# Kernel optimization log

Measured on AMD Instinct MI355X. Metric: run time of the kernel, lower is better.

## Reference

```python
import jax, jax.numpy as jnp
import numpy as np

B, N, DIN, DOUT = 8, 2048, 128, 128

def setup_inputs() -> dict:
    key = jax.random.key(0)
    k1, k2, k3, k4 = jax.random.split(key, 4)
    x = jax.random.normal(k1, (B, N, DIN), dtype=jnp.float32)
    adj = jax.random.uniform(k2, (B, N, N), dtype=jnp.float32)
    W = jax.random.normal(k3, (DIN, DOUT), dtype=jnp.float32) / np.sqrt(DIN)
    b = jax.random.normal(k4, (DOUT,), dtype=jnp.float32) * 0.01
    return {"x": x, "adj": adj, "W": W, "b": b}

def reference(x, adj, W, b):
    # degree over last dim of adj: [B, N]
    degree = jnp.sum(adj, axis=2)
    d_norm = 1.0 / jnp.sqrt(degree + 1e-8)
    # D^{-1/2} A D^{-1/2} == row/col elementwise scaling (same math as diag_embed+bmm)
    adj_norm = d_norm[:, :, None] * adj * d_norm[:, None, :]
    support = jnp.einsum('bnm,bmd->bnd', adj_norm, x)  # [B, N, DIN]
    return support @ W + b  # [B, N, DOUT]
```

## Files before the change

### kernel.cpp

```cpp
#include <hip/hip_runtime.h>
#include <hip/hip_bf16.h>

#define NN 2048
#define DD 128

typedef __attribute__((ext_vector_type(4))) float f32x4;
typedef __attribute__((ext_vector_type(8))) short short8;
typedef __attribute__((ext_vector_type(2))) unsigned int u32x2;

__device__ __forceinline__ unsigned short f2bf_bits(float f) {
  union { __hip_bfloat16 h; unsigned short s; } u;
  u.h = __float2bfloat16(f);
  return u.s;
}

__device__ __forceinline__ short8 cvt8(f32x4 a, f32x4 b) {
  short8 r;
  r[0] = (short)f2bf_bits(a[0]); r[1] = (short)f2bf_bits(a[1]);
  r[2] = (short)f2bf_bits(a[2]); r[3] = (short)f2bf_bits(a[3]);
  r[4] = (short)f2bf_bits(b[0]); r[5] = (short)f2bf_bits(b[1]);
  r[6] = (short)f2bf_bits(b[2]); r[7] = (short)f2bf_bits(b[3]);
  return r;
}

__device__ __forceinline__ void gld16(const void* src, void* lds) {
  __builtin_amdgcn_global_load_lds(
      (const __attribute__((address_space(1))) void*)src,
      (__attribute__((address_space(3))) void*)lds, 16, 0, 0);
}

__global__ void k_degcvt(const float* __restrict__ adj, float* __restrict__ dnorm,
                         short* __restrict__ adjS) {
  const int wv = threadIdx.x >> 6;
  const int ln = threadIdx.x & 63;
  const int row = blockIdx.x * 4 + wv;
  const f32x4* rowp = (const f32x4*)(adj + (size_t)row * NN);
  f32x4 v[8];
  float s = 0.0f;
#pragma unroll
  for (int i = 0; i < 8; ++i) {
    v[i] = rowp[i * 64 + ln];
    s += v[i][0] + v[i][1] + v[i][2] + v[i][3];
  }
#pragma unroll
  for (int off = 32; off >= 1; off >>= 1) s += __shfl_xor(s, off);
  const float dn = rsqrtf(s + 1e-8f);
  if (ln == 0) dnorm[row] = dn;
  u32x2* orow = (u32x2*)(adjS + (size_t)row * NN);
#pragma unroll
  for (int i = 0; i < 8; ++i) {
    u32x2 u;
    u[0] = (unsigned)f2bf_bits(v[i][0] * dn) | ((unsigned)f2bf_bits(v[i][1] * dn) << 16);
    u[1] = (unsigned)f2bf_bits(v[i][2] * dn) | ((unsigned)f2bf_bits(v[i][3] * dn) << 16);
    orow[i * 64 + ln] = u;
  }
}

__global__ void k_y(const float* __restrict__ x, const float* __restrict__ W,
                    const float* __restrict__ dnorm, short* __restrict__ yT) {
  const int ln = threadIdx.x & 63;
  const int wv = threadIdx.x >> 6;
  const int bb = blockIdx.x >> 5;
  const int n0 = (blockIdx.x & 31) << 6;
  const int l15 = ln & 15, l4 = ln >> 4;
  const int dbase = wv * 32;

  short8 af[2][4];
#pragma unroll
  for (int dt = 0; dt < 2; ++dt)
#pragma unroll
    for (int ks = 0; ks < 4; ++ks) {
      short8 a;
#pragma unroll
      for (int j = 0; j < 8; ++j)
        a[j] = (short)f2bf_bits(W[(size_t)(ks * 32 + l4 * 8 + j) * DD + dbase + dt * 16 + l15]);
      af[dt][ks] = a;
    }

  f32x4 acc[2][4];
#pragma unroll
  for (int dt = 0; dt < 2; ++dt)
#pragma unroll
    for (int nt = 0; nt < 4; ++nt) acc[dt][nt] = (f32x4)0.0f;

  const float* xb = x + (size_t)bb * NN * DD;
  const float* dnb = dnorm + (size_t)bb * NN;
#pragma unroll
  for (int nt = 0; nt < 4; ++nt) {
    const int n = n0 + nt * 16 + l15;
    const float dn = dnb[n];
#pragma unroll
    for (int ks = 0; ks < 4; ++ks) {
      f32x4 p = *(const f32x4*)(xb + (size_t)n * DD + ks * 32 + l4 * 8);
      f32x4 q = *(const f32x4*)(xb + (size_t)n * DD + ks * 32 + l4 * 8 + 4);
      short8 bf = cvt8(p * dn, q * dn);
#pragma unroll
      for (int dt = 0; dt < 2; ++dt)
        acc[dt][nt] = __builtin_amdgcn_mfma_f32_16x16x32_bf16(af[dt][ks], bf, acc[dt][nt], 0, 0, 0);
    }
  }

  short* yb = yT + (size_t)bb * DD * NN;
#pragma unroll
  for (int dt = 0; dt < 2; ++dt)
#pragma unroll
    for (int nt = 0; nt < 4; ++nt)
#pragma unroll
      for (int r = 0; r < 4; ++r) {
        int d = dbase + dt * 16 + l4 * 4 + r;
        yb[(size_t)d * NN + n0 + nt * 16 + l15] = (short)f2bf_bits(acc[dt][nt][r]);
      }
}

__launch_bounds__(512, 1)
__global__ void k_gemm(const short* __restrict__ adjS, const short* __restrict__ yT,
                       const float* __restrict__ bias, float* __restrict__ out) {
  __shared__ short As[6][4096];

  const int t = threadIdx.x;
  const int ln = t & 63;
  const int wv = t >> 6;
  const int orig = ((blockIdx.x & 7) << 5) | (blockIdx.x >> 3);
  const int bb = orig >> 5;
  const int m0 = (orig & 31) << 6;

  const char* ablk = (const char*)(adjS + ((size_t)bb * NN + m0) * NN);
  const int oc = (wv << 4) + (ln & 15);
  const int kg8 = (ln >> 4) << 3;
  const short* ybase = yT + ((size_t)bb * DD + oc) * NN;

  f32x4 acc[4];
#pragma unroll
  for (int m = 0; m < 4; ++m) acc[m] = (f32x4)0.0f;

  auto stage = [&](int tile, int buf) {
    unsigned L = (unsigned)t << 4;
    unsigned row = L >> 7;
    unsigned off = L & 127u;
    unsigned soff = off ^ ((row & 7u) << 4);
    const char* src = ablk + (size_t)row * (NN * 2) + (size_t)tile * 128 + soff;
    gld16(src, (char*)As + buf * 8192 + L);
  };
  auto loadB = [&](int tile, int ks) {
    return *(const short8*)(ybase + tile * 64 + ks * 32 + kg8);
  };
  auto compute = [&](int buf, short8 bk0, short8 bk1) {
    const char* base = (const char*)As + buf * 8192;
#pragma unroll
    for (int ks = 0; ks < 2; ++ks) {
      short8 bf = ks ? bk1 : bk0;
#pragma unroll
      for (int m = 0; m < 4; ++m) {
        unsigned row = (unsigned)(m * 16 + (ln & 15));
        unsigned c = (unsigned)(ks * 64 + (ln >> 4) * 16);
        short8 a = *(const short8*)(base + (row << 7) + (c ^ ((row & 7u) << 4)));
        acc[m] = __builtin_amdgcn_mfma_f32_16x16x32_bf16(a, bf, acc[m], 0, 0, 0);
      }
    }
  };

#pragma unroll
  for (int p = 0; p < 5; ++p) stage(p, p);
  short8 b0k0 = loadB(0, 0), b0k1 = loadB(0, 1);
  short8 b1k0 = loadB(1, 0), b1k1 = loadB(1, 1);
  asm volatile("s_waitcnt vmcnt(0)\n\ts_barrier" ::: "memory");

  int cbuf = 0, sbuf = 5;
  for (int tt = 0; tt < 32; tt += 2) {
    stage((tt + 5) & 31, sbuf);
    short8 n0k0 = loadB((tt + 2) & 31, 0), n0k1 = loadB((tt + 2) & 31, 1);
    compute(cbuf, b0k0, b0k1);
    asm volatile("s_waitcnt vmcnt(12)\n\ts_barrier" ::: "memory");
    cbuf = (cbuf == 5) ? 0 : cbuf + 1;
    sbuf = (sbuf == 5) ? 0 : sbuf + 1;
    stage((tt + 6) & 31, sbuf);
    short8 n1k0 = loadB((tt + 3) & 31, 0), n1k1 = loadB((tt + 3) & 31, 1);
    compute(cbuf, b1k0, b1k1);
    asm volatile("s_waitcnt vmcnt(12)\n\ts_barrier" ::: "memory");
    cbuf = (cbuf == 5) ? 0 : cbuf + 1;
    sbuf = (sbuf == 5) ? 0 : sbuf + 1;
    b0k0 = n0k0; b0k1 = n0k1; b1k0 = n1k0; b1k1 = n1k1;
  }

  const float bv = bias[oc];
  const int rbase = (ln >> 4) << 2;
#pragma unroll
  for (int m = 0; m < 4; ++m)
#pragma unroll
    for (int r = 0; r < 4; ++r)
      out[(size_t)(bb * NN + m0 + m * 16 + rbase + r) * DD + oc] = acc[m][r] + bv;
}

extern "C" void kernel_launch(void* const* d_in, const int* in_sizes, int n_in,
                              void* d_out, int out_size, void* d_ws, size_t ws_size,
                              hipStream_t stream) {
  (void)in_sizes; (void)n_in; (void)out_size; (void)ws_size;
  const float* x = (const float*)d_in[0];
  const float* adj = (const float*)d_in[1];
  const float* W = (const float*)d_in[2];
  const float* bias = (const float*)d_in[3];
  float* out = (float*)d_out;

  char* ws = (char*)d_ws;
  float* dnorm = (float*)ws;
  short* yT = (short*)(ws + (1 << 16));
  short* adjS = (short*)(ws + (1 << 16) + (4 << 20));

  k_degcvt<<<4096, 256, 0, stream>>>(adj, dnorm, adjS);
  k_y<<<256, 256, 0, stream>>>(x, W, dnorm, yT);
  k_gemm<<<256, 512, 0, stream>>>(adjS, yT, bias, out);
}
```

Before: 71.91 us.

## Fuse adj bf16 conversion into GEMM and apply row normalization in epilogue

Drops the intermediate bf16 copy of the normalized adjacency. The degree kernel now only computes d^{-1/2}, and the GEMM reads fp32 adj directly, converts it to bf16 while writing LDS, and applies row scaling to the output. This removes a 64MB write plus its reread, at the cost of reading fp32 adj twice and a register-staged, per-tile-barrier pipeline with smaller 32-row tiles and more blocks.

```diff
diff --git a/kernel.cpp b/kernel.cpp
--- a/kernel.cpp
+++ b/kernel.cpp
@@ -23,37 +23,20 @@
   return r;
 }
 
-__device__ __forceinline__ void gld16(const void* src, void* lds) {
-  __builtin_amdgcn_global_load_lds(
-      (const __attribute__((address_space(1))) void*)src,
-      (__attribute__((address_space(3))) void*)lds, 16, 0, 0);
-}
-
-__global__ void k_degcvt(const float* __restrict__ adj, float* __restrict__ dnorm,
-                         short* __restrict__ adjS) {
+__global__ void k_degree(const float* __restrict__ adj, float* __restrict__ dnorm) {
   const int wv = threadIdx.x >> 6;
   const int ln = threadIdx.x & 63;
   const int row = blockIdx.x * 4 + wv;
   const f32x4* rowp = (const f32x4*)(adj + (size_t)row * NN);
-  f32x4 v[8];
   float s = 0.0f;
 #pragma unroll
   for (int i = 0; i < 8; ++i) {
-    v[i] = rowp[i * 64 + ln];
-    s += v[i][0] + v[i][1] + v[i][2] + v[i][3];
+    f32x4 v = rowp[i * 64 + ln];
+    s += v[0] + v[1] + v[2] + v[3];
   }
 #pragma unroll
   for (int off = 32; off >= 1; off >>= 1) s += __shfl_xor(s, off);
-  const float dn = rsqrtf(s + 1e-8f);
-  if (ln == 0) dnorm[row] = dn;
-  u32x2* orow = (u32x2*)(adjS + (size_t)row * NN);
-#pragma unroll
-  for (int i = 0; i < 8; ++i) {
-    u32x2 u;
-    u[0] = (unsigned)f2bf_bits(v[i][0] * dn) | ((unsigned)f2bf_bits(v[i][1] * dn) << 16);
-    u[1] = (unsigned)f2bf_bits(v[i][2] * dn) | ((unsigned)f2bf_bits(v[i][3] * dn) << 16);
-    orow[i * 64 + ln] = u;
-  }
+  if (ln == 0) dnorm[row] = rsqrtf(s + 1e-8f);
 }
 
 __global__ void k_y(const float* __restrict__ x, const float* __restrict__ W,
@@ -112,83 +95,94 @@
       }
 }
 
-__launch_bounds__(512, 1)
-__global__ void k_gemm(const short* __restrict__ adjS, const short* __restrict__ yT,
-                       const float* __restrict__ bias, float* __restrict__ out) {
-  __shared__ short As[6][4096];
+__launch_bounds__(512, 4)
+__global__ void k_gemm(const float* __restrict__ adj, const short* __restrict__ yT,
+                       const float* __restrict__ dnorm, const float* __restrict__ bias,
+                       float* __restrict__ out) {
+  __shared__ short As[4][2048];
 
   const int t = threadIdx.x;
   const int ln = t & 63;
   const int wv = t >> 6;
-  const int orig = ((blockIdx.x & 7) << 5) | (blockIdx.x >> 3);
-  const int bb = orig >> 5;
-  const int m0 = (orig & 31) << 6;
-
-  const char* ablk = (const char*)(adjS + ((size_t)bb * NN + m0) * NN);
+  const int orig = ((blockIdx.x & 7) << 6) | (blockIdx.x >> 3);
+  const int bb = orig >> 6;
+  const int m0 = (orig & 63) << 5;
+
+  const float* ablk = adj + ((size_t)bb * NN + m0) * NN;
   const int oc = (wv << 4) + (ln & 15);
   const int kg8 = (ln >> 4) << 3;
   const short* ybase = yT + ((size_t)bb * DD + oc) * NN;
 
-  f32x4 acc[4];
-#pragma unroll
-  for (int m = 0; m < 4; ++m) acc[m] = (f32x4)0.0f;
-
-  auto stage = [&](int tile, int buf) {
-    unsigned L = (unsigned)t << 4;
-    unsigned row = L >> 7;
-    unsigned off = L & 127u;
-    unsigned soff = off ^ ((row & 7u) << 4);
-    const char* src = ablk + (size_t)row * (NN * 2) + (size_t)tile * 128 + soff;
-    gld16(src, (char*)As + buf * 8192 + L);
-  };
-  auto loadB = [&](int tile, int ks) {
-    return *(const short8*)(ybase + tile * 64 + ks * 32 + kg8);
-  };
-  auto compute = [&](int buf, short8 bk0, short8 bk1) {
-    const char* base = (const char*)As + buf * 8192;
+  const unsigned srow = (unsigned)t >> 4;
+  const unsigned sc4 = ((unsigned)t & 15u) << 2;
+
+  f32x4 acc[2];
+  acc[0] = (f32x4)0.0f; acc[1] = (f32x4)0.0f;
+
+  auto loadA = [&](int tile) -> f32x4 {
+    return *(const f32x4*)(ablk + (size_t)srow * NN + ((tile & 31) << 6) + sc4);
+  };
+  auto loadB = [&](int tile, int ks) -> short8 {
+    return *(const short8*)(ybase + ((tile & 31) << 6) + ks * 32 + kg8);
+  };
+  auto writeA = [&](f32x4 v, int buf) {
+    unsigned byte = (srow << 7) + (sc4 << 1);
+    byte ^= (srow & 7u) << 4;
+    u32x2 u;
+    u[0] = (unsigned)f2bf_bits(v[0]) | ((unsigned)f2bf_bits(v[1]) << 16);
+    u[1] = (unsigned)f2bf_bits(v[2]) | ((unsigned)f2bf_bits(v[3]) << 16);
+    *(u32x2*)((char*)As + (buf << 12) + byte) = u;
+  };
+  auto compute = [&](int buf, short8 b0, short8 b1) {
+    const char* base = (const char*)As + (buf << 12);
 #pragma unroll
     for (int ks = 0; ks < 2; ++ks) {
-      short8 bf = ks ? bk1 : bk0;
-#pragma unroll
-      for (int m = 0; m < 4; ++m) {
+      short8 bf = ks ? b1 : b0;
+#pragma unroll
+      for (int m = 0; m < 2; ++m) {
         unsigned row = (unsigned)(m * 16 + (ln & 15));
-        unsigned c = (unsigned)(ks * 64 + (ln >> 4) * 16);
-        short8 a = *(const short8*)(base + (row << 7) + (c ^ ((row & 7u) << 4)));
+        unsigned byte = (row << 7) + (unsigned)((ks * 32 + kg8) << 1);
+        byte ^= (row & 7u) << 4;
+        short8 a = *(const short8*)(base + byte);
         acc[m] = __builtin_amdgcn_mfma_f32_16x16x32_bf16(a, bf, acc[m], 0, 0, 0);
       }
     }
   };
 
-#pragma unroll
-  for (int p = 0; p < 5; ++p) stage(p, p);
-  short8 b0k0 = loadB(0, 0), b0k1 = loadB(0, 1);
-  short8 b1k0 = loadB(1, 0), b1k1 = loadB(1, 1);
-  asm volatile("s_waitcnt vmcnt(0)\n\ts_barrier" ::: "memory");
-
-  int cbuf = 0, sbuf = 5;
-  for (int tt = 0; tt < 32; tt += 2) {
-    stage((tt + 5) & 31, sbuf);
-    short8 n0k0 = loadB((tt + 2) & 31, 0), n0k1 = loadB((tt + 2) & 31, 1);
-    compute(cbuf, b0k0, b0k1);
-    asm volatile("s_waitcnt vmcnt(12)\n\ts_barrier" ::: "memory");
-    cbuf = (cbuf == 5) ? 0 : cbuf + 1;
-    sbuf = (sbuf == 5) ? 0 : sbuf + 1;
-    stage((tt + 6) & 31, sbuf);
-    short8 n1k0 = loadB((tt + 3) & 31, 0), n1k1 = loadB((tt + 3) & 31, 1);
-    compute(cbuf, b1k0, b1k1);
-    asm volatile("s_waitcnt vmcnt(12)\n\ts_barrier" ::: "memory");
-    cbuf = (cbuf == 5) ? 0 : cbuf + 1;
-    sbuf = (sbuf == 5) ? 0 : sbuf + 1;
-    b0k0 = n0k0; b0k1 = n0k1; b1k0 = n1k0; b1k1 = n1k1;
-  }
+  f32x4 sA0 = loadA(0), sA1 = loadA(1), sA2 = loadA(2), sA3 = loadA(3);
+  short8 bE0 = loadB(0, 0), bE1 = loadB(0, 1);
+  short8 bO0 = loadB(1, 0), bO1 = loadB(1, 1);
+  writeA(sA0, 0);
+  asm volatile("s_waitcnt lgkmcnt(0)\n\ts_barrier" ::: "memory");
+
+#define GITER(T, SNEW, SWR, BC0, BC1)                                 \
+  {                                                                   \
+    SNEW = loadA((T) + 4);                                            \
+    short8 nb0 = loadB((T) + 2, 0), nb1 = loadB((T) + 2, 1);          \
+    writeA(SWR, ((T) + 1) & 3);                                       \
+    asm volatile("s_waitcnt lgkmcnt(0)\n\ts_barrier" ::: "memory");   \
+    compute((T) & 3, BC0, BC1);                                       \
+    BC0 = nb0; BC1 = nb1;                                             \
+  }
+
+#pragma unroll 1
+  for (int t4 = 0; t4 < 32; t4 += 4) {
+    GITER(t4 + 0, sA0, sA1, bE0, bE1);
+    GITER(t4 + 1, sA1, sA2, bO0, bO1);
+    GITER(t4 + 2, sA2, sA3, bE0, bE1);
+    GITER(t4 + 3, sA3, sA0, bO0, bO1);
+  }
+#undef GITER
 
   const float bv = bias[oc];
   const int rbase = (ln >> 4) << 2;
 #pragma unroll
-  for (int m = 0; m < 4; ++m)
+  for (int m = 0; m < 2; ++m) {
+    f32x4 dn = *(const f32x4*)(dnorm + (size_t)bb * NN + m0 + m * 16 + rbase);
 #pragma unroll
     for (int r = 0; r < 4; ++r)
-      out[(size_t)(bb * NN + m0 + m * 16 + rbase + r) * DD + oc] = acc[m][r] + bv;
+      out[(size_t)(bb * NN + m0 + m * 16 + rbase + r) * DD + oc] = acc[m][r] * dn[r] + bv;
+  }
 }
 
 extern "C" void kernel_launch(void* const* d_in, const int* in_sizes, int n_in,
@@ -204,9 +198,8 @@
   char* ws = (char*)d_ws;
   float* dnorm = (float*)ws;
   short* yT = (short*)(ws + (1 << 16));
-  short* adjS = (short*)(ws + (1 << 16) + (4 << 20));
-
-  k_degcvt<<<4096, 256, 0, stream>>>(adj, dnorm, adjS);
+
+  k_degree<<<4096, 256, 0, stream>>>(adj, dnorm);
   k_y<<<256, 256, 0, stream>>>(x, W, dnorm, yT);
-  k_gemm<<<256, 512, 0, stream>>>(adjS, yT, bias, out);
-}
+  k_gemm<<<512, 512, 0, stream>>>(adj, yT, dnorm, bias, out);
+}
```

After: 69.25 us. 3.7% less time.

## Fuse fp32-to-bf16 adjacency conversion into the GEMM and apply row scaling in epilogue

Applied to the files above, without the earlier changes.

Drops the intermediate bf16 scaled copy of the adjacency matrix. The degree kernel now only computes the normalization vector, and the GEMM streams fp32 adjacency tiles into LDS, converting to bf16 in registers before the MFMA. Row normalization is applied to the accumulator in the epilogue. This removes a large global write and re-read, but doubles the GEMM's adjacency read volume and LDS footprint and adds conversion work in the inner loop.

```diff
diff --git a/kernel.cpp b/kernel.cpp
--- a/kernel.cpp
+++ b/kernel.cpp
@@ -6,7 +6,6 @@
 
 typedef __attribute__((ext_vector_type(4))) float f32x4;
 typedef __attribute__((ext_vector_type(8))) short short8;
-typedef __attribute__((ext_vector_type(2))) unsigned int u32x2;
 
 __device__ __forceinline__ unsigned short f2bf_bits(float f) {
   union { __hip_bfloat16 h; unsigned short s; } u;
@@ -29,31 +28,20 @@
       (__attribute__((address_space(3))) void*)lds, 16, 0, 0);
 }
 
-__global__ void k_degcvt(const float* __restrict__ adj, float* __restrict__ dnorm,
-                         short* __restrict__ adjS) {
+__global__ void k_degree(const float* __restrict__ adj, float* __restrict__ dnorm) {
   const int wv = threadIdx.x >> 6;
   const int ln = threadIdx.x & 63;
   const int row = blockIdx.x * 4 + wv;
   const f32x4* rowp = (const f32x4*)(adj + (size_t)row * NN);
-  f32x4 v[8];
   float s = 0.0f;
 #pragma unroll
   for (int i = 0; i < 8; ++i) {
-    v[i] = rowp[i * 64 + ln];
-    s += v[i][0] + v[i][1] + v[i][2] + v[i][3];
+    f32x4 v = rowp[i * 64 + ln];
+    s += v[0] + v[1] + v[2] + v[3];
   }
 #pragma unroll
   for (int off = 32; off >= 1; off >>= 1) s += __shfl_xor(s, off);
-  const float dn = rsqrtf(s + 1e-8f);
-  if (ln == 0) dnorm[row] = dn;
-  u32x2* orow = (u32x2*)(adjS + (size_t)row * NN);
-#pragma unroll
-  for (int i = 0; i < 8; ++i) {
-    u32x2 u;
-    u[0] = (unsigned)f2bf_bits(v[i][0] * dn) | ((unsigned)f2bf_bits(v[i][1] * dn) << 16);
-    u[1] = (unsigned)f2bf_bits(v[i][2] * dn) | ((unsigned)f2bf_bits(v[i][3] * dn) << 16);
-    orow[i * 64 + ln] = u;
-  }
+  if (ln == 0) dnorm[row] = rsqrtf(s + 1e-8f);
 }
 
 __global__ void k_y(const float* __restrict__ x, const float* __restrict__ W,
@@ -106,16 +94,17 @@
 #pragma unroll
     for (int nt = 0; nt < 4; ++nt)
 #pragma unroll
-      for (int r = 0; r < 4; ++r) {
-        int d = dbase + dt * 16 + l4 * 4 + r;
-        yb[(size_t)d * NN + n0 + nt * 16 + l15] = (short)f2bf_bits(acc[dt][nt][r]);
+      for (int rr = 0; rr < 4; ++rr) {
+        int d = dbase + dt * 16 + l4 * 4 + rr;
+        yb[(size_t)d * NN + n0 + nt * 16 + l15] = (short)f2bf_bits(acc[dt][nt][rr]);
       }
 }
 
 __launch_bounds__(512, 1)
-__global__ void k_gemm(const short* __restrict__ adjS, const short* __restrict__ yT,
-                       const float* __restrict__ bias, float* __restrict__ out) {
-  __shared__ short As[6][4096];
+__global__ void k_gemm2(const float* __restrict__ adj, const short* __restrict__ yT,
+                        const float* __restrict__ dnorm, const float* __restrict__ bias,
+                        float* __restrict__ out) {
+  __shared__ float As[6][4096];
 
   const int t = threadIdx.x;
   const int ln = t & 63;
@@ -124,7 +113,7 @@
   const int bb = orig >> 5;
   const int m0 = (orig & 31) << 6;
 
-  const char* ablk = (const char*)(adjS + ((size_t)bb * NN + m0) * NN);
+  const char* ablk = (const char*)(adj + ((size_t)bb * NN + m0) * NN);
   const int oc = (wv << 4) + (ln & 15);
   const int kg8 = (ln >> 4) << 3;
   const short* ybase = yT + ((size_t)bb * DD + oc) * NN;
@@ -134,27 +123,32 @@
   for (int m = 0; m < 4; ++m) acc[m] = (f32x4)0.0f;
 
   auto stage = [&](int tile, int buf) {
-    unsigned L = (unsigned)t << 4;
-    unsigned row = L >> 7;
-    unsigned off = L & 127u;
-    unsigned soff = off ^ ((row & 7u) << 4);
-    const char* src = ablk + (size_t)row * (NN * 2) + (size_t)tile * 128 + soff;
-    gld16(src, (char*)As + buf * 8192 + L);
+#pragma unroll
+    for (int j = 0; j < 2; ++j) {
+      unsigned L = ((unsigned)j << 13) + ((unsigned)t << 4);
+      unsigned row = L >> 8;
+      unsigned off = L & 255u;
+      unsigned soff = off ^ ((row & 7u) << 4);
+      const char* src = ablk + (size_t)row * (NN * 4) + (size_t)tile * 256 + soff;
+      gld16(src, (char*)As + buf * 16384 + L);
+    }
   };
-  auto loadB = [&](int tile, int ks) {
-    return *(const short8*)(ybase + tile * 64 + ks * 32 + kg8);
+  auto loadB = [&](int tile, int ks) -> short8 {
+    return *(const short8*)(ybase + ((tile & 31) << 6) + ks * 32 + kg8);
   };
-  auto compute = [&](int buf, short8 bk0, short8 bk1) {
-    const char* base = (const char*)As + buf * 8192;
+  auto compute = [&](int buf, short8 b0, short8 b1) {
+    const char* base = (const char*)As + buf * 16384;
 #pragma unroll
     for (int ks = 0; ks < 2; ++ks) {
-      short8 bf = ks ? bk1 : bk0;
+      short8 bf = ks ? b1 : b0;
 #pragma unroll
       for (int m = 0; m < 4; ++m) {
         unsigned row = (unsigned)(m * 16 + (ln & 15));
-        unsigned c = (unsigned)(ks * 64 + (ln >> 4) * 16);
-        short8 a = *(const short8*)(base + (row << 7) + (c ^ ((row & 7u) << 4)));
-        acc[m] = __builtin_amdgcn_mfma_f32_16x16x32_bf16(a, bf, acc[m], 0, 0, 0);
+        unsigned c = (unsigned)(ks * 128 + (ln >> 4) * 32);
+        unsigned sw = (row & 7u) << 4;
+        f32x4 f0 = *(const f32x4*)(base + (row << 8) + (c ^ sw));
+        f32x4 f1 = *(const f32x4*)(base + (row << 8) + ((c + 16) ^ sw));
+        acc[m] = __builtin_amdgcn_mfma_f32_16x16x32_bf16(cvt8(f0, f1), bf, acc[m], 0, 0, 0);
       }
     }
   };
@@ -166,15 +160,16 @@
   asm volatile("s_waitcnt vmcnt(0)\n\ts_barrier" ::: "memory");
 
   int cbuf = 0, sbuf = 5;
+#pragma unroll 1
   for (int tt = 0; tt < 32; tt += 2) {
-    stage((tt + 5) & 31, sbuf);
-    short8 n0k0 = loadB((tt + 2) & 31, 0), n0k1 = loadB((tt + 2) & 31, 1);
+    if (tt + 5 < 32) stage(tt + 5, sbuf);
+    short8 n0k0 = loadB(tt + 2, 0), n0k1 = loadB(tt + 2, 1);
     compute(cbuf, b0k0, b0k1);
     asm volatile("s_waitcnt vmcnt(12)\n\ts_barrier" ::: "memory");
     cbuf = (cbuf == 5) ? 0 : cbuf + 1;
     sbuf = (sbuf == 5) ? 0 : sbuf + 1;
-    stage((tt + 6) & 31, sbuf);
-    short8 n1k0 = loadB((tt + 3) & 31, 0), n1k1 = loadB((tt + 3) & 31, 1);
+    if (tt + 6 < 32) stage(tt + 6, sbuf);
+    short8 n1k0 = loadB(tt + 3, 0), n1k1 = loadB(tt + 3, 1);
     compute(cbuf, b1k0, b1k1);
     asm volatile("s_waitcnt vmcnt(12)\n\ts_barrier" ::: "memory");
     cbuf = (cbuf == 5) ? 0 : cbuf + 1;
@@ -185,10 +180,12 @@
   const float bv = bias[oc];
   const int rbase = (ln >> 4) << 2;
 #pragma unroll
-  for (int m = 0; m < 4; ++m)
-#pragma unroll
-    for (int r = 0; r < 4; ++r)
-      out[(size_t)(bb * NN + m0 + m * 16 + rbase + r) * DD + oc] = acc[m][r] + bv;
+  for (int m = 0; m < 4; ++m) {
+    f32x4 dn = *(const f32x4*)(dnorm + (size_t)bb * NN + m0 + m * 16 + rbase);
+#pragma unroll
+    for (int rr = 0; rr < 4; ++rr)
+      out[(size_t)(bb * NN + m0 + m * 16 + rbase + rr) * DD + oc] = acc[m][rr] * dn[rr] + bv;
+  }
 }
 
 extern "C" void kernel_launch(void* const* d_in, const int* in_sizes, int n_in,
@@ -204,9 +201,8 @@
   char* ws = (char*)d_ws;
   float* dnorm = (float*)ws;
   short* yT = (short*)(ws + (1 << 16));
-  short* adjS = (short*)(ws + (1 << 16) + (4 << 20));
-
-  k_degcvt<<<4096, 256, 0, stream>>>(adj, dnorm, adjS);
+
+  k_degree<<<4096, 256, 0, stream>>>(adj, dnorm);
   k_y<<<256, 256, 0, stream>>>(x, W, dnorm, yT);
-  k_gemm<<<256, 512, 0, stream>>>(adjS, yT, bias, out);
-}
+  k_gemm2<<<256, 512, 0, stream>>>(adj, yT, dnorm, bias, out);
+}
```

New measurement: 67.93 us. 5.5% less time.
